# Kernel tuning notes

Hardware: AMD Instinct MI355X
Metric: run time of the kernel (lower is better)

The kernel has to match this reference:

```python
import jax, jax.numpy as jnp
import numpy as np

# Four fixed 3x3 'gradient' kernels (left, right, up, down), stacked as OIHW (4,1,3,3).
_K = np.zeros((4, 1, 3, 3), np.float32)
_K[0, 0, 1, 0] = -1.0; _K[0, 0, 1, 1] = 1.0   # left:  center - left neighbor
_K[1, 0, 1, 1] = 1.0;  _K[1, 0, 1, 2] = -1.0  # right: center - right neighbor
_K[2, 0, 0, 1] = -1.0; _K[2, 0, 1, 1] = 1.0   # up:    center - upper neighbor
_K[3, 0, 1, 1] = 1.0;  _K[3, 0, 2, 1] = -1.0  # down:  center - lower neighbor
KERNELS = jnp.asarray(_K)

LOSS_WEIGHT = 1.0
POOL = 4


def _avgpool4(x):
    # AvgPool2d(4) on NCHW with H,W divisible by 4
    b, c, h, w = x.shape
    return x.reshape(b, c, h // POOL, POOL, w // POOL, POOL).mean(axis=(3, 5))


def _grad_conv(x):
    # F.conv2d(x, kernels, padding=1); x: (B,1,Hp,Wp) -> (B,4,Hp,Wp)
    return jax.lax.conv_general_dilated(
        x, KERNELS, window_strides=(1, 1), padding=((1, 1), (1, 1)),
        dimension_numbers=('NCHW', 'OIHW', 'NCHW'))


def setup_inputs() -> dict:
    key = jax.random.key(0)
    k1, k2 = jax.random.split(key)
    B, C, H, W = 32, 3, 512, 512
    x = jax.random.uniform(k1, (B, C, H, W), dtype=jnp.float32)
    pred = jax.random.uniform(k2, (B, C, H, W), dtype=jnp.float32)
    return {"x": x, "pred": pred}


def reference(x, pred):
    # channel mean -> (B,1,H,W), then 4x4 average pool -> (B,1,H/4,W/4)
    org_pool = _avgpool4(jnp.mean(x, axis=1, keepdims=True))
    enh_pool = _avgpool4(jnp.mean(pred, axis=1, keepdims=True))
    # NOTE: the original computes weight_diff and E_1 but never uses them in the
    # returned loss, so they are omitted (no effect on output or gradients).
    d = _grad_conv(org_pool) - _grad_conv(enh_pool)  # (B,4,Hp,Wp)
    # mean(D_left + D_right + D_up + D_down) == mean over (B,Hp,Wp) of channel-sum
    E = jnp.mean(jnp.sum(d * d, axis=1))
    return LOSS_WEIGHT * E
```

## Files before the change

### kernel.cpp

```cpp
#include <hip/hip_runtime.h>

constexpr int B  = 32;
constexpr int C  = 3;
constexpr int H  = 512;
constexpr int W  = 512;
constexpr int HP = H / 4;
constexpr int WP = W / 4;
constexpr int NP = B * HP * WP;

constexpr int TX = 64;
constexpr int TY = 32;
constexpr int HX = TX + 1;
constexpr int HY = TY + 1;
constexpr int TILES_X = WP / TX;
constexpr int TILES_Y = HP / TY;
constexpr int NBLOCKS = B * TILES_X * TILES_Y;

__global__ __launch_bounds__(256) void spatial_loss_fused(
        const float* __restrict__ x,
        const float* __restrict__ pred,
        float* __restrict__ out) {
    __shared__ float pt[HY][HX];

    int blk = blockIdx.x;
    int b   = blk >> 3;
    int ty  = (blk >> 1) & 3;
    int tx  = blk & 1;
    int y0  = ty * TY;
    int x0  = tx * TX;
    int tid = threadIdx.x;

    for (int i = tid; i < HY * HX; i += 256) {
        int hy = i / HX;
        int hx = i - hy * HX;
        int gy = y0 + hy - 1;
        int gx = x0 + hx - 1;
        float s = 0.0f;
        if ((unsigned)gy < (unsigned)HP && (unsigned)gx < (unsigned)WP) {
            size_t base = (((size_t)b * C) * H + (size_t)gy * 4) * W + (size_t)gx * 4;
            #pragma unroll
            for (int c = 0; c < C; ++c) {
                const float4* xb = (const float4*)(x    + base + (size_t)c * H * W);
                const float4* pb = (const float4*)(pred + base + (size_t)c * H * W);
                #pragma unroll
                for (int r = 0; r < 4; ++r) {
                    float4 xv = xb[r * (W / 4)];
                    float4 pv = pb[r * (W / 4)];
                    s += (xv.x - pv.x) + (xv.y - pv.y) + (xv.z - pv.z) + (xv.w - pv.w);
                }
            }
            s *= (1.0f / 48.0f);
        }
        pt[hy][hx] = s;
    }
    __syncthreads();

    float acc = 0.0f;
    #pragma unroll
    for (int j = 0; j < (TY * TX) / 256; ++j) {
        int i  = tid + j * 256;
        int r  = i >> 6;
        int xx = i & 63;
        int gy = y0 + r;
        int gx = x0 + xx;
        float c  = pt[r + 1][xx + 1];
        float up = pt[r + 0][xx + 1];
        float lf = pt[r + 1][xx + 0];
        float dy = c - up;
        float dx = c - lf;
        float wy = (gy > 0) ? 2.0f : 1.0f;
        float wx = (gx > 0) ? 2.0f : 1.0f;
        acc += wy * dy * dy + wx * dx * dx;
        if (gy == HP - 1) acc += c * c;
        if (gx == WP - 1) acc += c * c;
    }

    #pragma unroll
    for (int off = 32; off > 0; off >>= 1)
        acc += __shfl_down(acc, off, 64);

    __shared__ float ws_red[4];
    int lane = tid & 63;
    int wid  = tid >> 6;
    if (lane == 0) ws_red[wid] = acc;
    __syncthreads();
    if (tid == 0) {
        float s = ws_red[0] + ws_red[1] + ws_red[2] + ws_red[3];
        atomicAdd(out, s * (1.0f / (float)NP));
    }
}

extern "C" void kernel_launch(void* const* d_in, const int* in_sizes, int n_in,
                              void* d_out, int out_size, void* d_ws, size_t ws_size,
                              hipStream_t stream) {
    const float* x    = (const float*)d_in[0];
    const float* pred = (const float*)d_in[1];
    float* out = (float*)d_out;

    hipMemsetAsync(out, 0, sizeof(float), stream);

    spatial_loss_fused<<<NBLOCKS, 256, 0, stream>>>(x, pred, out);
}
```

Before: 216.7 us.

## Restructure tiles to full-width row strips with coalesced float4 loads and block swizzle

Each block now covers 8 full-width pooled rows (all 128 columns) instead of a 32x64 tile with a 1-pixel halo on both axes. Each thread loads one float4 column across rows, so a wave reads contiguous 512-float rows. Only the row above is recomputed as halo, and the left neighbour comes from shared memory, which removes the column halo and the strided per-pixel loads. It also swizzles the block order across images and requests 2 blocks per CU. In exchange there are more blocks (512 vs 256), which means more atomics and more redundant halo-row reads.

```diff
diff --git a/kernel.cpp b/kernel.cpp
--- a/kernel.cpp
+++ b/kernel.cpp
@@ -7,72 +7,96 @@
 constexpr int HP = H / 4;
 constexpr int WP = W / 4;
 constexpr int NP = B * HP * WP;
+constexpr int W4 = W / 4;
 
-constexpr int TX = 64;
-constexpr int TY = 32;
-constexpr int HX = TX + 1;
-constexpr int HY = TY + 1;
-constexpr int TILES_X = WP / TX;
-constexpr int TILES_Y = HP / TY;
-constexpr int NBLOCKS = B * TILES_X * TILES_Y;
+constexpr int ROWS_PB    = 8;
+constexpr int BLK_PER_IMG = HP / ROWS_PB;
+constexpr int NBLOCKS    = B * BLK_PER_IMG;
 
-__global__ __launch_bounds__(256) void spatial_loss_fused(
+__global__ __launch_bounds__(256, 2) void spatial_loss_fused(
         const float* __restrict__ x,
         const float* __restrict__ pred,
         float* __restrict__ out) {
-    __shared__ float pt[HY][HX];
+    __shared__ float pt[ROWS_PB + 1][WP];
 
-    int blk = blockIdx.x;
-    int b   = blk >> 3;
-    int ty  = (blk >> 1) & 3;
-    int tx  = blk & 1;
-    int y0  = ty * TY;
-    int x0  = tx * TX;
-    int tid = threadIdx.x;
+    int orig = blockIdx.x;
+    int blk  = (orig & 7) * (NBLOCKS / 8) + (orig >> 3);
+    int b    = blk >> 4;
+    int br   = blk & 15;
+    int tid  = threadIdx.x;
+    int q    = tid & 127;
+    int h    = tid >> 7;
 
-    for (int i = tid; i < HY * HX; i += 256) {
-        int hy = i / HX;
-        int hx = i - hy * HX;
-        int gy = y0 + hy - 1;
-        int gx = x0 + hx - 1;
+    const float4* __restrict__ xb = (const float4*)x;
+    const float4* __restrict__ pb = (const float4*)pred;
+
+    int row0 = br * 32 + h * 16;
+    #pragma unroll
+    for (int j = 0; j < 4; ++j) {
+        int base = (b * C * H + row0 + 4 * j) * W4 + q;
+        float s0 = 0.0f, s1 = 0.0f;
+        #pragma unroll
+        for (int c = 0; c < C; ++c) {
+            int a = base + c * H * W4;
+            float4 x0 = xb[a];
+            float4 x1 = xb[a + W4];
+            float4 x2 = xb[a + 2 * W4];
+            float4 x3 = xb[a + 3 * W4];
+            float4 p0 = pb[a];
+            float4 p1 = pb[a + W4];
+            float4 p2 = pb[a + 2 * W4];
+            float4 p3 = pb[a + 3 * W4];
+            s0 += (x0.x - p0.x) + (x0.y - p0.y) + (x0.z - p0.z) + (x0.w - p0.w);
+            s1 += (x1.x - p1.x) + (x1.y - p1.y) + (x1.z - p1.z) + (x1.w - p1.w);
+            s0 += (x2.x - p2.x) + (x2.y - p2.y) + (x2.z - p2.z) + (x2.w - p2.w);
+            s1 += (x3.x - p3.x) + (x3.y - p3.y) + (x3.z - p3.z) + (x3.w - p3.w);
+        }
+        pt[1 + 4 * h + j][q] = (s0 + s1) * (1.0f / 48.0f);
+    }
+
+    if (tid < 128) {
         float s = 0.0f;
-        if ((unsigned)gy < (unsigned)HP && (unsigned)gx < (unsigned)WP) {
-            size_t base = (((size_t)b * C) * H + (size_t)gy * 4) * W + (size_t)gx * 4;
+        if (br > 0) {
+            int hr   = br * 32 - 4;
+            int base = (b * C * H + hr) * W4 + tid;
+            float s0 = 0.0f, s1 = 0.0f;
             #pragma unroll
             for (int c = 0; c < C; ++c) {
-                const float4* xb = (const float4*)(x    + base + (size_t)c * H * W);
-                const float4* pb = (const float4*)(pred + base + (size_t)c * H * W);
-                #pragma unroll
-                for (int r = 0; r < 4; ++r) {
-                    float4 xv = xb[r * (W / 4)];
-                    float4 pv = pb[r * (W / 4)];
-                    s += (xv.x - pv.x) + (xv.y - pv.y) + (xv.z - pv.z) + (xv.w - pv.w);
-                }
+                int a = base + c * H * W4;
+                float4 x0 = xb[a];
+                float4 x1 = xb[a + W4];
+                float4 x2 = xb[a + 2 * W4];
+                float4 x3 = xb[a + 3 * W4];
+                float4 p0 = pb[a];
+                float4 p1 = pb[a + W4];
+                float4 p2 = pb[a + 2 * W4];
+                float4 p3 = pb[a + 3 * W4];
+                s0 += (x0.x - p0.x) + (x0.y - p0.y) + (x0.z - p0.z) + (x0.w - p0.w);
+                s1 += (x1.x - p1.x) + (x1.y - p1.y) + (x1.z - p1.z) + (x1.w - p1.w);
+                s0 += (x2.x - p2.x) + (x2.y - p2.y) + (x2.z - p2.z) + (x2.w - p2.w);
+                s1 += (x3.x - p3.x) + (x3.y - p3.y) + (x3.z - p3.z) + (x3.w - p3.w);
             }
-            s *= (1.0f / 48.0f);
+            s = (s0 + s1) * (1.0f / 48.0f);
         }
-        pt[hy][hx] = s;
+        pt[0][tid] = s;
     }
     __syncthreads();
 
     float acc = 0.0f;
     #pragma unroll
-    for (int j = 0; j < (TY * TX) / 256; ++j) {
-        int i  = tid + j * 256;
-        int r  = i >> 6;
-        int xx = i & 63;
-        int gy = y0 + r;
-        int gx = x0 + xx;
-        float c  = pt[r + 1][xx + 1];
-        float up = pt[r + 0][xx + 1];
-        float lf = pt[r + 1][xx + 0];
+    for (int j = 0; j < 4; ++j) {
+        int row = 4 * h + j;
+        int gy  = br * 8 + row;
+        float c  = pt[row + 1][q];
+        float up = pt[row][q];
+        float lf = (q > 0) ? pt[row + 1][q - 1] : 0.0f;
         float dy = c - up;
         float dx = c - lf;
         float wy = (gy > 0) ? 2.0f : 1.0f;
-        float wx = (gx > 0) ? 2.0f : 1.0f;
+        float wx = (q  > 0) ? 2.0f : 1.0f;
         acc += wy * dy * dy + wx * dx * dx;
         if (gy == HP - 1) acc += c * c;
-        if (gx == WP - 1) acc += c * c;
+        if (q  == WP - 1) acc += c * c;
     }
 
     #pragma unroll
```

Result: no change. 219.9 us (+1.5%).
